# Kernel tuning notes

Measured on AMD Instinct MI355X. Metric: run time of the kernel, lower is better.

Reference implementation:

```python
import jax, jax.numpy as jnp
import numpy as np

H = 512   # hidden_dim
O = 128   # output_dim
S = 512   # max_seq_len
B = 256   # batch


def setup_inputs() -> dict:
    key = jax.random.key(0)
    ks = jax.random.split(key, 10)
    sc_ih = 1.0 / np.sqrt(H)
    inp = {
        "C": jax.random.normal(ks[0], (B, H), dtype=jnp.float32),
        "t": jax.random.uniform(ks[1], (S, B, 1), dtype=jnp.float32),
        "mask": jnp.ones((S, B), dtype=bool),
        # nn.LSTM(2H, H) params (PyTorch layout: [4H, in], gate order i,f,g,o)
        "W_ih": jax.random.uniform(ks[2], (4 * H, 2 * H), minval=-sc_ih, maxval=sc_ih),
        "W_hh": jax.random.uniform(ks[3], (4 * H, H), minval=-sc_ih, maxval=sc_ih),
        "b_ih": jax.random.uniform(ks[4], (4 * H,), minval=-sc_ih, maxval=sc_ih),
        "b_hh": jax.random.uniform(ks[5], (4 * H,), minval=-sc_ih, maxval=sc_ih),
        # nn.Linear(H, O)
        "lin_W": jax.random.uniform(ks[6], (O, H), minval=-sc_ih, maxval=sc_ih),
        "lin_b": jax.random.uniform(ks[7], (O,), minval=-sc_ih, maxval=sc_ih),
        # nn.Linear(1, H)
        "time_W": jax.random.uniform(ks[8], (H, 1), minval=-1.0, maxval=1.0),
        "time_b": jax.random.uniform(ks[9], (H,), minval=-1.0, maxval=1.0),
    }
    return inp


def _forward(C, t, W_ih, W_hh, b_ih, b_hh, lin_W, lin_b, time_W, time_b):
    # time deltas, first delta = 0   -> [S, B, 1]
    t_delta = t[1:] - t[:-1]
    t_delta_mat = jnp.concatenate([jnp.zeros_like(t_delta[0:1]), t_delta], axis=0)
    # time_lin: [S, B, H]
    time_encoded = t_delta_mat[:, :, 0:1] @ time_W.T + time_b
    # per-step LSTM input: concat(C, time_encoded[s])  -> [S, B, 2H]
    x = jnp.concatenate(
        [jnp.broadcast_to(C[None], (t.shape[0], C.shape[0], C.shape[1])), time_encoded],
        axis=-1,
    )
    # precompute input-to-gate projections in one big GEMM: [S, B, 4H]
    xg = jnp.einsum("sbi,gi->sbg", x, W_ih) + b_ih + b_hh
    Hd = C.shape[1]

    def step(carry, xg_t):
        h, c = carry
        gates = xg_t + h @ W_hh.T
        i, f, g, o = jnp.split(gates, 4, axis=-1)
        c = jax.nn.sigmoid(f) * c + jax.nn.sigmoid(i) * jnp.tanh(g)
        h = jax.nn.sigmoid(o) * jnp.tanh(c)
        return (h, c), h

    h0 = jnp.zeros((C.shape[0], Hd), dtype=C.dtype)
    _, hs = jax.lax.scan(step, (h0, h0), xg)   # hs: [S, B, H]
    return hs @ lin_W.T + lin_b                # [S, B, O]


def reference(C, t, mask, W_ih, W_hh, b_ih, b_hh, lin_W, lin_b, time_W, time_b):
    # mask is accepted by the original forward but never used
    return _forward(C, t, W_ih, W_hh, b_ih, b_hh, lin_W, lin_b, time_W, time_b)
```

## Files before the change

kernel.cpp:

```cpp
#include <hip/hip_runtime.h>
#include <stdint.h>


#define HD 512
#define BD 256
#define SD 512
#define OD 128
#define SENT 0xFF80FF80u

typedef __attribute__((ext_vector_type(8))) short short8;
typedef __attribute__((ext_vector_type(4))) float f32x4;
typedef __attribute__((ext_vector_type(4))) unsigned int u32x4;

static __device__ __forceinline__ unsigned short f2bf(float x) {
  unsigned int u = __float_as_uint(x);
  u += 0x7fffu + ((u >> 16) & 1u);
  return (unsigned short)(u >> 16);
}
static __device__ __forceinline__ float sigm(float x) {
  return 1.0f / (1.0f + __expf(-x));
}
static __device__ __forceinline__ float tanhf_(float x) {
  x = fminf(15.f, fmaxf(-15.f, x));
  float e = __expf(2.f * x);
  return (e - 1.f) / (e + 1.f);
}
static __device__ __forceinline__ int badchk(u32x4 v) {
  return (v.x == SENT) | (v.y == SENT) | (v.z == SENT) | (v.w == SENT);
}

__global__ __launch_bounds__(256) void k_cvt(const float* __restrict__ whh,
                                             const float* __restrict__ linw,
                                             unsigned short* __restrict__ whhb,
                                             unsigned short* __restrict__ linwb) {
  int i = blockIdx.x * 256 + threadIdx.x;
  whhb[i] = f2bf(whh[i]);
  if (i < OD * HD) linwb[i] = f2bf(linw[i]);
}

__global__ __launch_bounds__(256) void k_td(const float* __restrict__ t,
                                            float* __restrict__ td) {
  int i = blockIdx.x * 256 + threadIdx.x;
  float v = 0.f;
  if (i >= BD) v = t[i] - t[i - BD];
  td[i] = v;
}

__global__ __launch_bounds__(256) void k_u(const float* __restrict__ wih,
                                           const float* __restrict__ tw,
                                           const float* __restrict__ tb,
                                           const float* __restrict__ bih,
                                           const float* __restrict__ bhh,
                                           float* __restrict__ u,
                                           float* __restrict__ ub) {
  int gc = blockIdx.x * 256 + threadIdx.x;
  const float4* w4 = (const float4*)(wih + (size_t)gc * (2 * HD) + HD);
  const float4* t4 = (const float4*)tw;
  const float4* b4 = (const float4*)tb;
  float a = 0.f, b = 0.f;
  for (int k = 0; k < HD / 4; ++k) {
    float4 w = w4[k], tv = t4[k], bv = b4[k];
    a += w.x * tv.x + w.y * tv.y + w.z * tv.z + w.w * tv.w;
    b += w.x * bv.x + w.y * bv.y + w.z * bv.z + w.w * bv.w;
  }
  u[gc] = a;
  ub[gc] = b + bih[gc] + bhh[gc];
}

__global__ __launch_bounds__(1024) void k_cw(const float* __restrict__ C,
                                             const float* __restrict__ wih,
                                             const float* __restrict__ ub,
                                             float* __restrict__ CW) {
  int gc = blockIdx.x * 64 + (threadIdx.x & 63);
  int b  = blockIdx.y * 16 + (threadIdx.x >> 6);
  const float4* c4 = (const float4*)(C + (size_t)b * HD);
  const float4* w4 = (const float4*)(wih + (size_t)gc * (2 * HD));
  float acc = 0.f;
  for (int k = 0; k < HD / 4; ++k) {
    float4 cv = c4[k], wv = w4[k];
    acc += cv.x * wv.x + cv.y * wv.y + cv.z * wv.z + cv.w * wv.w;
  }
  CW[(size_t)b * (4 * HD) + gc] = acc + ub[gc];
}

__global__ __launch_bounds__(256) void k_poison(unsigned int* __restrict__ hbuf) {
  u32x4 s = {SENT, SENT, SENT, SENT};
  unsigned int* p = hbuf + (size_t)(blockIdx.x * 256 + threadIdx.x) * 4;
  asm volatile("global_store_dwordx4 %0, %1, off sc0 sc1" :: "v"(p), "v"(s) : "memory");
}

__global__ __launch_bounds__(256, 1) void k_main(
    const float* __restrict__ CW, const float* __restrict__ u,
    const float* __restrict__ td, const unsigned short* __restrict__ whhb,
    const unsigned short* __restrict__ linwb, const float* __restrict__ linb,
    unsigned short* __restrict__ hbuf, float* __restrict__ out)
{
  __shared__ __align__(16) unsigned short hlds[16 * HD];
  __shared__ __align__(16) unsigned short lwlds[16 * HD];
  __shared__ float gbuf[4][16][33];

  const int tid  = threadIdx.x;
  const int lane = tid & 63;
  const int wv   = tid >> 6;
  const int gid  = blockIdx.x & 15;
  const int m    = blockIdx.x >> 4;

  short8 w0[16], w1[16];
  {
    const unsigned short* wb =
        whhb + ((size_t)wv * HD + m * 32 + (lane & 15)) * HD + (lane >> 4) * 8;
    #pragma unroll
    for (int kk = 0; kk < 16; ++kk) {
      asm volatile("global_load_dwordx4 %0, %2, off\n\t"
                   "global_load_dwordx4 %1, %3, off"
                   : "=&v"(w0[kk]), "=&v"(w1[kk])
                   : "v"(wb + kk * 32), "v"(wb + 16 * HD + kk * 32) : "memory");
    }
  }

  if (m < 8) {
    for (int i = tid; i < 16 * 64; i += 256) {
      int rl = i >> 6, c = i & 63;
      *(short8*)((char*)lwlds + (size_t)rl * 1024 + (size_t)c * 16) =
          *(const short8*)((const char*)linwb + (size_t)(m * 16 + rl) * 1024 +
                           (size_t)((c ^ (rl & 7)) * 16));
    }
  }

  const int r    = tid >> 4;
  const int jl0  = (tid & 15) * 2;
  const int grow = gid * 16 + r;
  const int col0 = m * 32 + jl0;
  const int foff = r * 1024 + (((col0 >> 3) ^ (r & 7)) << 4) + ((col0 * 2) & 15);
  float cwr[8], ur[8];
  #pragma unroll
  for (int g = 0; g < 4; ++g) {
    int col = g * HD + col0;
    cwr[g * 2]     = CW[(size_t)grow * (4 * HD) + col];
    cwr[g * 2 + 1] = CW[(size_t)grow * (4 * HD) + col + 1];
    ur[g * 2]      = u[col];
    ur[g * 2 + 1]  = u[col + 1];
  }
  float cs0 = 0.f, cs1 = 0.f;

  const int  wsel  = 1 + (m % 3);
  const bool owsel = (m < 8) && (wv == wsel);
  float lb = 0.f;
  if (m < 8) lb = linb[m * 16 + (lane & 15)];

  char* hb = (char*)hbuf + (size_t)gid * 49152;

  const int arow  = lane & 15;
  const int akoff = lane >> 4;
  const int axor  = arow & 7;
  const int lrow  = lane & 15;
  const int lxor  = (lrow & 7) << 4;

  u32x4 v0, v1, v2, v3;
  float tdn = 0.f, tdv = 0.f;

  asm volatile("s_waitcnt vmcnt(0)" ::: "memory");
  __builtin_amdgcn_sched_barrier(0);
  __syncthreads();

  for (int t = 0; t < SD; ++t) {
    const size_t oN = (size_t)((t + 1) % 3) * 16384;
    const size_t oR = (size_t)(t % 3) * 16384;

    f32x4 acc0 = {0.f, 0.f, 0.f, 0.f}, acc1 = {0.f, 0.f, 0.f, 0.f};
    if (t > 0) {
      #pragma unroll
      for (int kk = 0; kk < 16; ++kk) {
        short8 a = *(const short8*)((const char*)hlds + (size_t)arow * 1024 +
                                    (size_t)(((kk * 4 + akoff) ^ axor) << 4));
        acc0 = __builtin_amdgcn_mfma_f32_16x16x32_bf16(a, w0[kk], acc0, 0, 0, 0);
        acc1 = __builtin_amdgcn_mfma_f32_16x16x32_bf16(a, w1[kk], acc1, 0, 0, 0);
      }
    }
    {
      int rr = (lane >> 4) * 4, cc = lane & 15;
      #pragma unroll
      for (int qq = 0; qq < 4; ++qq) {
        gbuf[wv][rr + qq][cc]      = acc0[qq];
        gbuf[wv][rr + qq][16 + cc] = acc1[qq];
      }
    }
    asm volatile("s_waitcnt lgkmcnt(0)" ::: "memory");
    __builtin_amdgcn_s_barrier();

    unsigned int hp;
    {
      float p0i = gbuf[0][r][jl0]     + cwr[0] + tdv * ur[0];
      float p1i = gbuf[0][r][jl0 + 1] + cwr[1] + tdv * ur[1];
      float p0f = gbuf[1][r][jl0]     + cwr[2] + tdv * ur[2];
      float p1f = gbuf[1][r][jl0 + 1] + cwr[3] + tdv * ur[3];
      float p0g = gbuf[2][r][jl0]     + cwr[4] + tdv * ur[4];
      float p1g = gbuf[2][r][jl0 + 1] + cwr[5] + tdv * ur[5];
      float p0o = gbuf[3][r][jl0]     + cwr[6] + tdv * ur[6];
      float p1o = gbuf[3][r][jl0 + 1] + cwr[7] + tdv * ur[7];
      cs0 = sigm(p0f) * cs0 + sigm(p0i) * tanhf_(p0g);
      cs1 = sigm(p1f) * cs1 + sigm(p1i) * tanhf_(p1g);
      float h0 = sigm(p0o) * tanhf_(cs0);
      float h1 = sigm(p1o) * tanhf_(cs1);
      hp = (unsigned int)f2bf(h0) | ((unsigned int)f2bf(h1) << 16);
    }

    {
      char* hsl = hb + oN + foff;
      asm volatile("global_store_dword %0, %1, off sc0 sc1" :: "v"(hsl), "v"(hp) : "memory");
    }

    {
      const char* src = hb + oN + (size_t)tid * 16;
      asm volatile(
          "global_load_dwordx4 %0, %4, off sc0 sc1\n\t"
          "global_load_dwordx4 %1, %5, off sc0 sc1\n\t"
          "global_load_dwordx4 %2, %6, off sc0 sc1\n\t"
          "global_load_dwordx4 %3, %7, off sc0 sc1"
          : "=&v"(v0), "=&v"(v1), "=&v"(v2), "=&v"(v3)
          : "v"(src), "v"(src + 4096), "v"(src + 8192), "v"(src + 12288)
          : "memory");
      int tt = (t + 1 < SD) ? (t + 1) : t;
      const float* ta = td + (size_t)tt * BD + grow;
      asm volatile("global_load_dword %0, %1, off" : "=&v"(tdn) : "v"(ta) : "memory");
    }

    if (owsel && t > 0) {
      f32x4 osA = {0.f, 0.f, 0.f, 0.f}, osB = {0.f, 0.f, 0.f, 0.f};
      #pragma unroll
      for (int kk = 0; kk < 8; ++kk) {
        short8 aA = *(const short8*)((const char*)hlds + (size_t)arow * 1024 +
                                     (size_t)(((kk * 4 + akoff) ^ axor) << 4));
        short8 aB = *(const short8*)((const char*)hlds + (size_t)arow * 1024 +
                                     (size_t)((((kk + 8) * 4 + akoff) ^ axor) << 4));
        short8 bA = *(const short8*)((const char*)lwlds + (size_t)lrow * 1024 +
                                     (size_t)((kk * 64 + akoff * 16) ^ lxor));
        short8 bB = *(const short8*)((const char*)lwlds + (size_t)lrow * 1024 +
                                     (size_t)(((kk + 8) * 64 + akoff * 16) ^ lxor));
        osA = __builtin_amdgcn_mfma_f32_16x16x32_bf16(aA, bA, osA, 0, 0, 0);
        osB = __builtin_amdgcn_mfma_f32_16x16x32_bf16(aB, bB, osB, 0, 0, 0);
      }
      float* ob = out + (size_t)(t - 1) * (BD * OD) + (size_t)(gid * 16) * OD + m * 16;
      int rr = (lane >> 4) * 4, cc = lane & 15;
      #pragma unroll
      for (int qq = 0; qq < 4; ++qq) {
        float vst = osA[qq] + osB[qq] + lb;
        float* oa = ob + (size_t)(rr + qq) * OD + cc;
        asm volatile("global_store_dword %0, %1, off" :: "v"(oa), "v"(vst) : "memory");
      }
    } else {
      __builtin_amdgcn_s_sleep(13);
    }

    asm volatile("s_waitcnt vmcnt(0)" ::: "memory");
    __builtin_amdgcn_sched_barrier(0);
    {
      int p0 = badchk(v0), p1 = badchk(v1), p2 = badchk(v2), p3 = badchk(v3);
      int guard = 0;
      while (p0 | p1 | p2 | p3) {
        if (++guard > (1 << 16)) break;
        __builtin_amdgcn_s_sleep(2);
        const char* src = hb + oN + (size_t)tid * 16;
        if (p0) asm volatile("global_load_dwordx4 %0, %1, off sc0 sc1" : "=&v"(v0) : "v"(src) : "memory");
        if (p1) asm volatile("global_load_dwordx4 %0, %1, off sc0 sc1" : "=&v"(v1) : "v"(src + 4096) : "memory");
        if (p2) asm volatile("global_load_dwordx4 %0, %1, off sc0 sc1" : "=&v"(v2) : "v"(src + 8192) : "memory");
        if (p3) asm volatile("global_load_dwordx4 %0, %1, off sc0 sc1" : "=&v"(v3) : "v"(src + 12288) : "memory");
        asm volatile("s_waitcnt vmcnt(0)" ::: "memory");
        __builtin_amdgcn_sched_barrier(0);
        p0 = badchk(v0); p1 = badchk(v1); p2 = badchk(v2); p3 = badchk(v3);
      }
    }

    {
      char* pp = hb + oR + (size_t)m * 1024 + (size_t)tid * 4;
      unsigned int s = SENT;
      asm volatile("global_store_dword %0, %1, off sc0 sc1" :: "v"(pp), "v"(s) : "memory");
    }

    __builtin_amdgcn_s_barrier();

    *(u32x4*)((char*)hlds + (size_t)tid * 16)         = v0;
    *(u32x4*)((char*)hlds + 4096 + (size_t)tid * 16)  = v1;
    *(u32x4*)((char*)hlds + 8192 + (size_t)tid * 16)  = v2;
    *(u32x4*)((char*)hlds + 12288 + (size_t)tid * 16) = v3;
    asm volatile("s_waitcnt lgkmcnt(0)" ::: "memory");
    __builtin_amdgcn_s_barrier();

    tdv = tdn;
  }

  if (owsel) {
    f32x4 osA = {0.f, 0.f, 0.f, 0.f}, osB = {0.f, 0.f, 0.f, 0.f};
    #pragma unroll
    for (int kk = 0; kk < 8; ++kk) {
      short8 aA = *(const short8*)((const char*)hlds + (size_t)arow * 1024 +
                                   (size_t)(((kk * 4 + akoff) ^ axor) << 4));
      short8 aB = *(const short8*)((const char*)hlds + (size_t)arow * 1024 +
                                   (size_t)((((kk + 8) * 4 + akoff) ^ axor) << 4));
      short8 bA = *(const short8*)((const char*)lwlds + (size_t)lrow * 1024 +
                                   (size_t)((kk * 64 + akoff * 16) ^ lxor));
      short8 bB = *(const short8*)((const char*)lwlds + (size_t)lrow * 1024 +
                                   (size_t)(((kk + 8) * 64 + akoff * 16) ^ lxor));
      osA = __builtin_amdgcn_mfma_f32_16x16x32_bf16(aA, bA, osA, 0, 0, 0);
      osB = __builtin_amdgcn_mfma_f32_16x16x32_bf16(aB, bB, osB, 0, 0, 0);
    }
    float* ob = out + (size_t)(SD - 1) * (BD * OD) + (size_t)(gid * 16) * OD + m * 16;
    int rr = (lane >> 4) * 4, cc = lane & 15;
    #pragma unroll
    for (int qq = 0; qq < 4; ++qq) {
      float vst = osA[qq] + osB[qq] + lb;
      float* oa = ob + (size_t)(rr + qq) * OD + cc;
      asm volatile("global_store_dword %0, %1, off" :: "v"(oa), "v"(vst) : "memory");
    }
  }
}

extern "C" void kernel_launch(void* const* d_in, const int* in_sizes, int n_in,
                              void* d_out, int out_size, void* d_ws, size_t ws_size,
                              hipStream_t stream) {
  const float* C    = (const float*)d_in[0];
  const float* t    = (const float*)d_in[1];
  const float* Wih  = (const float*)d_in[3];
  const float* Whh  = (const float*)d_in[4];
  const float* bih  = (const float*)d_in[5];
  const float* bhh  = (const float*)d_in[6];
  const float* linW = (const float*)d_in[7];
  const float* linb = (const float*)d_in[8];
  const float* tW   = (const float*)d_in[9];
  const float* tb   = (const float*)d_in[10];
  float* out = (float*)d_out;

  char* ws = (char*)d_ws;
  float*          CW    = (float*)(ws + 0);
  float*          u     = (float*)(ws + 2097152);
  float*          ub    = (float*)(ws + 2105344);
  float*          td    = (float*)(ws + 2113536);
  unsigned short* whhb  = (unsigned short*)(ws + 2637824);
  unsigned short* linwb = (unsigned short*)(ws + 4734976);
  unsigned short* hbuf  = (unsigned short*)(ws + 4866048);
  if (ws_size < 5652480) return;

  k_poison<<<192, 256, 0, stream>>>((unsigned int*)hbuf);
  k_cvt<<<4096, 256, 0, stream>>>(Whh, linW, whhb, linwb);
  k_td <<<512, 256, 0, stream>>>(t, td);
  k_u  <<<8, 256, 0, stream>>>(Wih, tW, tb, bih, bhh, u, ub);
  k_cw <<<dim3(32, 16), 1024, 0, stream>>>(C, Wih, ub, CW);
  k_main<<<256, 256, 0, stream>>>(CW, u, td, whhb, linwb, linb, hbuf, out);
}
```

Baseline: 1.856 ms.

## Stream h chunks directly from global into MFMA operands, split K across waves

Each wave now handles two gates over half of K, so partial gate sums are reduced through LDS. The wave loads its slice of the shared h-state straight from the global exchange buffer into registers in eight chunks, waiting on each chunk with a graded vmcnt so MFMAs start before the whole vector arrives. This removes the LDS staging of h and one barrier per step. The output projection is split across two waves and its store deferred by a step through a double-buffered LDS tile. It also reorders the sentinel reset, which adds per-chunk polling and more complex cross-block synchronisation.

```diff
diff --git a/kernel.cpp b/kernel.cpp
--- a/kernel.cpp
+++ b/kernel.cpp
@@ -25,9 +25,12 @@
   float e = __expf(2.f * x);
   return (e - 1.f) / (e + 1.f);
 }
-static __device__ __forceinline__ int badchk(u32x4 v) {
-  return (v.x == SENT) | (v.y == SENT) | (v.z == SENT) | (v.w == SENT);
-}
+static __device__ __forceinline__ int badchk8(short8 v) {
+  u32x4 w;
+  __builtin_memcpy(&w, &v, 16);
+  return (w.x == SENT) | (w.y == SENT) | (w.z == SENT) | (w.w == SENT);
+}
+#define KEEPALIVE(x) asm volatile("" : "+v"(x))
 
 __global__ __launch_bounds__(256) void k_cvt(const float* __restrict__ whh,
                                              const float* __restrict__ linw,
@@ -95,9 +98,9 @@
     const unsigned short* __restrict__ linwb, const float* __restrict__ linb,
     unsigned short* __restrict__ hbuf, float* __restrict__ out)
 {
-  __shared__ __align__(16) unsigned short hlds[16 * HD];
+  __shared__ float gbufP[4][2][16][33];
+  __shared__ float obufP[2][2][16][16];
   __shared__ __align__(16) unsigned short lwlds[16 * HD];
-  __shared__ float gbuf[4][16][33];
 
   const int tid  = threadIdx.x;
   const int lane = tid & 63;
@@ -105,16 +108,25 @@
   const int gid  = blockIdx.x & 15;
   const int m    = blockIdx.x >> 4;
 
-  short8 w0[16], w1[16];
+  const int ga    = (wv >> 1) * 2;
+  const int khalf = wv & 1;
+
+  short8 wA0[8], wA1[8], wB0[8], wB1[8];
   {
-    const unsigned short* wb =
-        whhb + ((size_t)wv * HD + m * 32 + (lane & 15)) * HD + (lane >> 4) * 8;
-    #pragma unroll
-    for (int kk = 0; kk < 16; ++kk) {
-      asm volatile("global_load_dwordx4 %0, %2, off\n\t"
-                   "global_load_dwordx4 %1, %3, off"
-                   : "=&v"(w0[kk]), "=&v"(w1[kk])
-                   : "v"(wb + kk * 32), "v"(wb + 16 * HD + kk * 32) : "memory");
+    #pragma unroll
+    for (int j = 0; j < 8; ++j) {
+      size_t ko = (size_t)((khalf * 8 + j) * 32 + (lane >> 4) * 8);
+      const unsigned short* pA0 =
+          whhb + (size_t)(ga * HD + m * 32 + (lane & 15)) * HD + ko;
+      const unsigned short* pB0 = pA0 + (size_t)HD * HD;
+      asm volatile(
+          "global_load_dwordx4 %0, %4, off\n\t"
+          "global_load_dwordx4 %1, %5, off\n\t"
+          "global_load_dwordx4 %2, %6, off\n\t"
+          "global_load_dwordx4 %3, %7, off"
+          : "=&v"(wA0[j]), "=&v"(wA1[j]), "=&v"(wB0[j]), "=&v"(wB1[j])
+          : "v"(pA0), "v"(pA0 + 16 * HD), "v"(pB0), "v"(pB0 + 16 * HD)
+          : "memory");
     }
   }
 
@@ -131,7 +143,6 @@
   const int jl0  = (tid & 15) * 2;
   const int grow = gid * 16 + r;
   const int col0 = m * 32 + jl0;
-  const int foff = r * 1024 + (((col0 >> 3) ^ (r & 7)) << 4) + ((col0 * 2) & 15);
   float cwr[8], ur[8];
   #pragma unroll
   for (int g = 0; g < 4; ++g) {
@@ -142,9 +153,6 @@
     ur[g * 2 + 1]  = u[col + 1];
   }
   float cs0 = 0.f, cs1 = 0.f;
-
-  const int  wsel  = 1 + (m % 3);
-  const bool owsel = (m < 8) && (wv == wsel);
   float lb = 0.f;
   if (m < 8) lb = linb[m * 16 + (lane & 15)];
 
@@ -152,52 +160,106 @@
 
   const int arow  = lane & 15;
   const int akoff = lane >> 4;
-  const int axor  = arow & 7;
+  const int aoff  = arow * 64 + akoff * 16;
   const int lrow  = lane & 15;
   const int lxor  = (lrow & 7) << 4;
-
-  u32x4 v0, v1, v2, v3;
-  float tdn = 0.f, tdv = 0.f;
-
+  const int rr    = (lane >> 4) * 4;
+  const int cc    = lane & 15;
+
+  short8 a0{}, a1{}, a2{}, a3{}, a4{}, a5{}, a6{}, a7{};
+  float  tdn = 0.f;
+
+  #pragma unroll
+  for (int i = 0; i < 8; ++i) { KEEPALIVE(cwr[i]); KEEPALIVE(ur[i]); }
+  KEEPALIVE(lb);
   asm volatile("s_waitcnt vmcnt(0)" ::: "memory");
   __builtin_amdgcn_sched_barrier(0);
   __syncthreads();
 
+#define RETRY_CHUNK(J)                                                        \
+  {                                                                           \
+    int bad = badchk8(a##J);                                                  \
+    int guard = 0;                                                            \
+    while (__any(bad)) {                                                      \
+      if (++guard > (1 << 16)) break;                                         \
+      __builtin_amdgcn_s_sleep(2);                                            \
+      if (bad)                                                                \
+        asm volatile("global_load_dwordx4 %0, %1, off sc0 sc1"               \
+                     : "=&v"(a##J) : "v"(csrc + (J) * 1024) : "memory");      \
+      asm volatile("s_waitcnt vmcnt(0)" ::: "memory");                        \
+      __builtin_amdgcn_sched_barrier(0);                                      \
+      bad = badchk8(a##J);                                                    \
+    }                                                                         \
+  }
+
+#define GATE_CHUNK(J, REMSTR)                                                 \
+  {                                                                           \
+    asm volatile("s_waitcnt vmcnt(" REMSTR ")" ::: "memory");                 \
+    __builtin_amdgcn_sched_barrier(0);                                        \
+    RETRY_CHUNK(J)                                                            \
+    accA0 = __builtin_amdgcn_mfma_f32_16x16x32_bf16(a##J, wA0[J], accA0, 0, 0, 0); \
+    accA1 = __builtin_amdgcn_mfma_f32_16x16x32_bf16(a##J, wA1[J], accA1, 0, 0, 0); \
+    accB0 = __builtin_amdgcn_mfma_f32_16x16x32_bf16(a##J, wB0[J], accB0, 0, 0, 0); \
+    accB1 = __builtin_amdgcn_mfma_f32_16x16x32_bf16(a##J, wB1[J], accB1, 0, 0, 0); \
+  }
+
+#define OP_CHUNK(J)                                                           \
+  {                                                                           \
+    short8 bf = *(const short8*)((const char*)lwlds + (size_t)lrow * 1024 +   \
+        (size_t)((((khalf * 8 + (J)) * 64 + akoff * 16)) ^ lxor));            \
+    os = __builtin_amdgcn_mfma_f32_16x16x32_bf16(a##J, bf, os, 0, 0, 0);      \
+  }
+
+#define ISSUE_CHUNK(J)                                                        \
+  asm volatile("global_load_dwordx4 %0, %1, off sc0 sc1"                      \
+               : "=&v"(a##J) : "v"(nsrc + (J) * 1024) : "memory");
+
   for (int t = 0; t < SD; ++t) {
+    const size_t oC = (size_t)(t % 3) * 16384;
     const size_t oN = (size_t)((t + 1) % 3) * 16384;
-    const size_t oR = (size_t)(t % 3) * 16384;
-
-    f32x4 acc0 = {0.f, 0.f, 0.f, 0.f}, acc1 = {0.f, 0.f, 0.f, 0.f};
+    const size_t oR = (size_t)((t + 2) % 3) * 16384;
+
+    f32x4 accA0 = {0.f, 0.f, 0.f, 0.f}, accA1 = {0.f, 0.f, 0.f, 0.f};
+    f32x4 accB0 = {0.f, 0.f, 0.f, 0.f}, accB1 = {0.f, 0.f, 0.f, 0.f};
     if (t > 0) {
-      #pragma unroll
-      for (int kk = 0; kk < 16; ++kk) {
-        short8 a = *(const short8*)((const char*)hlds + (size_t)arow * 1024 +
-                                    (size_t)(((kk * 4 + akoff) ^ axor) << 4));
-        acc0 = __builtin_amdgcn_mfma_f32_16x16x32_bf16(a, w0[kk], acc0, 0, 0, 0);
-        acc1 = __builtin_amdgcn_mfma_f32_16x16x32_bf16(a, w1[kk], acc1, 0, 0, 0);
-      }
-    }
-    {
-      int rr = (lane >> 4) * 4, cc = lane & 15;
-      #pragma unroll
-      for (int qq = 0; qq < 4; ++qq) {
-        gbuf[wv][rr + qq][cc]      = acc0[qq];
-        gbuf[wv][rr + qq][16 + cc] = acc1[qq];
-      }
+      const char* csrc = hb + oC + (size_t)(khalf * 8) * 1024 + aoff;
+      GATE_CHUNK(0, "7")
+      GATE_CHUNK(1, "6")
+      GATE_CHUNK(2, "5")
+      GATE_CHUNK(3, "4")
+      GATE_CHUNK(4, "3")
+      GATE_CHUNK(5, "2")
+      GATE_CHUNK(6, "1")
+      GATE_CHUNK(7, "0")
+    }
+
+    #pragma unroll
+    for (int qq = 0; qq < 4; ++qq) {
+      gbufP[wv][0][rr + qq][cc]      = accA0[qq];
+      gbufP[wv][0][rr + qq][16 + cc] = accA1[qq];
+      gbufP[wv][1][rr + qq][cc]      = accB0[qq];
+      gbufP[wv][1][rr + qq][16 + cc] = accB1[qq];
     }
     asm volatile("s_waitcnt lgkmcnt(0)" ::: "memory");
     __builtin_amdgcn_s_barrier();
 
+    {
+      char* pp = hb + oR + (size_t)m * 1024 + (size_t)tid * 4;
+      unsigned int s = SENT;
+      asm volatile("global_store_dword %0, %1, off sc0 sc1" :: "v"(pp), "v"(s) : "memory");
+    }
+
     unsigned int hp;
     {
-      float p0i = gbuf[0][r][jl0]     + cwr[0] + tdv * ur[0];
-      float p1i = gbuf[0][r][jl0 + 1] + cwr[1] + tdv * ur[1];
-      float p0f = gbuf[1][r][jl0]     + cwr[2] + tdv * ur[2];
-      float p1f = gbuf[1][r][jl0 + 1] + cwr[3] + tdv * ur[3];
-      float p0g = gbuf[2][r][jl0]     + cwr[4] + tdv * ur[4];
-      float p1g = gbuf[2][r][jl0 + 1] + cwr[5] + tdv * ur[5];
-      float p0o = gbuf[3][r][jl0]     + cwr[6] + tdv * ur[6];
-      float p1o = gbuf[3][r][jl0 + 1] + cwr[7] + tdv * ur[7];
+      float tdv = (t > 0) ? tdn : 0.f;
+      float p0i = gbufP[0][0][r][jl0]     + gbufP[1][0][r][jl0]     + cwr[0] + tdv * ur[0];
+      float p1i = gbufP[0][0][r][jl0 + 1] + gbufP[1][0][r][jl0 + 1] + cwr[1] + tdv * ur[1];
+      float p0f = gbufP[0][1][r][jl0]     + gbufP[1][1][r][jl0]     + cwr[2] + tdv * ur[2];
+      float p1f = gbufP[0][1][r][jl0 + 1] + gbufP[1][1][r][jl0 + 1] + cwr[3] + tdv * ur[3];
+      float p0g = gbufP[2][0][r][jl0]     + gbufP[3][0][r][jl0]     + cwr[4] + tdv * ur[4];
+      float p1g = gbufP[2][0][r][jl0 + 1] + gbufP[3][0][r][jl0 + 1] + cwr[5] + tdv * ur[5];
+      float p0o = gbufP[2][1][r][jl0]     + gbufP[3][1][r][jl0]     + cwr[6] + tdv * ur[6];
+      float p1o = gbufP[2][1][r][jl0 + 1] + gbufP[3][1][r][jl0 + 1] + cwr[7] + tdv * ur[7];
       cs0 = sigm(p0f) * cs0 + sigm(p0i) * tanhf_(p0g);
       cs1 = sigm(p1f) * cs1 + sigm(p1i) * tanhf_(p1g);
       float h0 = sigm(p0o) * tanhf_(cs0);
@@ -206,111 +268,76 @@
     }
 
     {
-      char* hsl = hb + oN + foff;
+      char* hsl = hb + oN + (size_t)m * 1024 + (size_t)(r * 64 + jl0 * 2);
       asm volatile("global_store_dword %0, %1, off sc0 sc1" :: "v"(hsl), "v"(hp) : "memory");
     }
 
-    {
-      const char* src = hb + oN + (size_t)tid * 16;
-      asm volatile(
-          "global_load_dwordx4 %0, %4, off sc0 sc1\n\t"
-          "global_load_dwordx4 %1, %5, off sc0 sc1\n\t"
-          "global_load_dwordx4 %2, %6, off sc0 sc1\n\t"
-          "global_load_dwordx4 %3, %7, off sc0 sc1"
-          : "=&v"(v0), "=&v"(v1), "=&v"(v2), "=&v"(v3)
-          : "v"(src), "v"(src + 4096), "v"(src + 8192), "v"(src + 12288)
-          : "memory");
+    const char* nsrc = hb + oN + (size_t)(khalf * 8) * 1024 + aoff;
+    if (m < 8 && wv >= 2 && t > 0) {
+      f32x4 os = {0.f, 0.f, 0.f, 0.f};
+      OP_CHUNK(0) OP_CHUNK(1) OP_CHUNK(2) OP_CHUNK(3)
+      OP_CHUNK(4) OP_CHUNK(5) OP_CHUNK(6) OP_CHUNK(7)
+      #pragma unroll
+      for (int qq = 0; qq < 4; ++qq)
+        obufP[t & 1][khalf][rr + qq][cc] = os[qq];
       int tt = (t + 1 < SD) ? (t + 1) : t;
       const float* ta = td + (size_t)tt * BD + grow;
       asm volatile("global_load_dword %0, %1, off" : "=&v"(tdn) : "v"(ta) : "memory");
-    }
-
-    if (owsel && t > 0) {
-      f32x4 osA = {0.f, 0.f, 0.f, 0.f}, osB = {0.f, 0.f, 0.f, 0.f};
-      #pragma unroll
-      for (int kk = 0; kk < 8; ++kk) {
-        short8 aA = *(const short8*)((const char*)hlds + (size_t)arow * 1024 +
-                                     (size_t)(((kk * 4 + akoff) ^ axor) << 4));
-        short8 aB = *(const short8*)((const char*)hlds + (size_t)arow * 1024 +
-                                     (size_t)((((kk + 8) * 4 + akoff) ^ axor) << 4));
-        short8 bA = *(const short8*)((const char*)lwlds + (size_t)lrow * 1024 +
-                                     (size_t)((kk * 64 + akoff * 16) ^ lxor));
-        short8 bB = *(const short8*)((const char*)lwlds + (size_t)lrow * 1024 +
-                                     (size_t)(((kk + 8) * 64 + akoff * 16) ^ lxor));
-        osA = __builtin_amdgcn_mfma_f32_16x16x32_bf16(aA, bA, osA, 0, 0, 0);
-        osB = __builtin_amdgcn_mfma_f32_16x16x32_bf16(aB, bB, osB, 0, 0, 0);
+      ISSUE_CHUNK(0) ISSUE_CHUNK(1) ISSUE_CHUNK(2) ISSUE_CHUNK(3)
+      ISSUE_CHUNK(4) ISSUE_CHUNK(5) ISSUE_CHUNK(6) ISSUE_CHUNK(7)
+    } else {
+      __builtin_amdgcn_s_sleep(4);
+      if (m < 8 && wv == 0 && t >= 2) {
+        float* ob = out + (size_t)(t - 2) * (BD * OD) + (size_t)(gid * 16) * OD + m * 16;
+        #pragma unroll
+        for (int qq = 0; qq < 4; ++qq) {
+          float v = obufP[(t - 1) & 1][0][rr + qq][cc] +
+                    obufP[(t - 1) & 1][1][rr + qq][cc] + lb;
+          float* oa = ob + (size_t)(rr + qq) * OD + cc;
+          asm volatile("global_store_dword %0, %1, off" :: "v"(oa), "v"(v) : "memory");
+        }
       }
-      float* ob = out + (size_t)(t - 1) * (BD * OD) + (size_t)(gid * 16) * OD + m * 16;
-      int rr = (lane >> 4) * 4, cc = lane & 15;
-      #pragma unroll
-      for (int qq = 0; qq < 4; ++qq) {
-        float vst = osA[qq] + osB[qq] + lb;
-        float* oa = ob + (size_t)(rr + qq) * OD + cc;
-        asm volatile("global_store_dword %0, %1, off" :: "v"(oa), "v"(vst) : "memory");
-      }
-    } else {
-      __builtin_amdgcn_s_sleep(13);
-    }
-
+      int tt = (t + 1 < SD) ? (t + 1) : t;
+      const float* ta = td + (size_t)tt * BD + grow;
+      asm volatile("global_load_dword %0, %1, off" : "=&v"(tdn) : "v"(ta) : "memory");
+      ISSUE_CHUNK(0) ISSUE_CHUNK(1) ISSUE_CHUNK(2) ISSUE_CHUNK(3)
+      ISSUE_CHUNK(4) ISSUE_CHUNK(5) ISSUE_CHUNK(6) ISSUE_CHUNK(7)
+    }
+  }
+
+  __syncthreads();
+  if (m < 8 && wv == 0) {
+    float* ob = out + (size_t)(SD - 2) * (BD * OD) + (size_t)(gid * 16) * OD + m * 16;
+    #pragma unroll
+    for (int qq = 0; qq < 4; ++qq) {
+      float v = obufP[(SD - 1) & 1][0][rr + qq][cc] +
+                obufP[(SD - 1) & 1][1][rr + qq][cc] + lb;
+      float* oa = ob + (size_t)(rr + qq) * OD + cc;
+      asm volatile("global_store_dword %0, %1, off" :: "v"(oa), "v"(v) : "memory");
+    }
+  }
+  if (m < 8 && wv >= 2) {
+    const char* csrc = hb + (size_t)(SD % 3) * 16384 + (size_t)(khalf * 8) * 1024 + aoff;
     asm volatile("s_waitcnt vmcnt(0)" ::: "memory");
     __builtin_amdgcn_sched_barrier(0);
-    {
-      int p0 = badchk(v0), p1 = badchk(v1), p2 = badchk(v2), p3 = badchk(v3);
-      int guard = 0;
-      while (p0 | p1 | p2 | p3) {
-        if (++guard > (1 << 16)) break;
-        __builtin_amdgcn_s_sleep(2);
-        const char* src = hb + oN + (size_t)tid * 16;
-        if (p0) asm volatile("global_load_dwordx4 %0, %1, off sc0 sc1" : "=&v"(v0) : "v"(src) : "memory");
-        if (p1) asm volatile("global_load_dwordx4 %0, %1, off sc0 sc1" : "=&v"(v1) : "v"(src + 4096) : "memory");
-        if (p2) asm volatile("global_load_dwordx4 %0, %1, off sc0 sc1" : "=&v"(v2) : "v"(src + 8192) : "memory");
-        if (p3) asm volatile("global_load_dwordx4 %0, %1, off sc0 sc1" : "=&v"(v3) : "v"(src + 12288) : "memory");
-        asm volatile("s_waitcnt vmcnt(0)" ::: "memory");
-        __builtin_amdgcn_sched_barrier(0);
-        p0 = badchk(v0); p1 = badchk(v1); p2 = badchk(v2); p3 = badchk(v3);
-      }
-    }
-
-    {
-      char* pp = hb + oR + (size_t)m * 1024 + (size_t)tid * 4;
-      unsigned int s = SENT;
-      asm volatile("global_store_dword %0, %1, off sc0 sc1" :: "v"(pp), "v"(s) : "memory");
-    }
-
-    __builtin_amdgcn_s_barrier();
-
-    *(u32x4*)((char*)hlds + (size_t)tid * 16)         = v0;
-    *(u32x4*)((char*)hlds + 4096 + (size_t)tid * 16)  = v1;
-    *(u32x4*)((char*)hlds + 8192 + (size_t)tid * 16)  = v2;
-    *(u32x4*)((char*)hlds + 12288 + (size_t)tid * 16) = v3;
-    asm volatile("s_waitcnt lgkmcnt(0)" ::: "memory");
-    __builtin_amdgcn_s_barrier();
-
-    tdv = tdn;
-  }
-
-  if (owsel) {
-    f32x4 osA = {0.f, 0.f, 0.f, 0.f}, osB = {0.f, 0.f, 0.f, 0.f};
-    #pragma unroll
-    for (int kk = 0; kk < 8; ++kk) {
-      short8 aA = *(const short8*)((const char*)hlds + (size_t)arow * 1024 +
-                                   (size_t)(((kk * 4 + akoff) ^ axor) << 4));
-      short8 aB = *(const short8*)((const char*)hlds + (size_t)arow * 1024 +
-                                   (size_t)((((kk + 8) * 4 + akoff) ^ axor) << 4));
-      short8 bA = *(const short8*)((const char*)lwlds + (size_t)lrow * 1024 +
-                                   (size_t)((kk * 64 + akoff * 16) ^ lxor));
-      short8 bB = *(const short8*)((const char*)lwlds + (size_t)lrow * 1024 +
-                                   (size_t)(((kk + 8) * 64 + akoff * 16) ^ lxor));
-      osA = __builtin_amdgcn_mfma_f32_16x16x32_bf16(aA, bA, osA, 0, 0, 0);
-      osB = __builtin_amdgcn_mfma_f32_16x16x32_bf16(aB, bB, osB, 0, 0, 0);
-    }
+    RETRY_CHUNK(0) RETRY_CHUNK(1) RETRY_CHUNK(2) RETRY_CHUNK(3)
+    RETRY_CHUNK(4) RETRY_CHUNK(5) RETRY_CHUNK(6) RETRY_CHUNK(7)
+    f32x4 os = {0.f, 0.f, 0.f, 0.f};
+    OP_CHUNK(0) OP_CHUNK(1) OP_CHUNK(2) OP_CHUNK(3)
+    OP_CHUNK(4) OP_CHUNK(5) OP_CHUNK(6) OP_CHUNK(7)
+    #pragma unroll
+    for (int qq = 0; qq < 4; ++qq)
+      obufP[SD & 1][khalf][rr + qq][cc] = os[qq];
+  }
+  __syncthreads();
+  if (m < 8 && wv == 0) {
     float* ob = out + (size_t)(SD - 1) * (BD * OD) + (size_t)(gid * 16) * OD + m * 16;
-    int rr = (lane >> 4) * 4, cc = lane & 15;
     #pragma unroll
     for (int qq = 0; qq < 4; ++qq) {
-      float vst = osA[qq] + osB[qq] + lb;
+      float v = obufP[SD & 1][0][rr + qq][cc] +
+                obufP[SD & 1][1][rr + qq][cc] + lb;
       float* oa = ob + (size_t)(rr + qq) * OD + cc;
-      asm volatile("global_store_dword %0, %1, off" :: "v"(oa), "v"(vst) : "memory");
+      asm volatile("global_store_dword %0, %1, off" :: "v"(oa), "v"(v) : "memory");
     }
   }
 }
```

Result: slower. 2.076 ms (+11.8%).

## Specialize waves for h exchange and double-buffer LDS hidden state

Applied to the files above, without the earlier changes.

Reworks the per-step cross-block exchange of the hidden state. Each block now gathers its new h tile in LDS and one wave writes it to global with wide stores and re-poisons the stale slot. Two waves poll for and load the peers' h into a double-buffered LDS copy, while another wave computes the output projection. The goal is fewer barriers and less serialized global traffic per timestep. The cost is more LDS, harder wait-count reasoning, and added risk in the sentinel-poll protocol.

```diff
diff --git a/kernel.cpp b/kernel.cpp
--- a/kernel.cpp
+++ b/kernel.cpp
@@ -25,9 +25,12 @@
   float e = __expf(2.f * x);
   return (e - 1.f) / (e + 1.f);
 }
-static __device__ __forceinline__ int badchk(u32x4 v) {
-  return (v.x == SENT) | (v.y == SENT) | (v.z == SENT) | (v.w == SENT);
-}
+static __device__ __forceinline__ int badchk8(short8 v) {
+  u32x4 w;
+  __builtin_memcpy(&w, &v, 16);
+  return (w.x == SENT) | (w.y == SENT) | (w.z == SENT) | (w.w == SENT);
+}
+#define KEEPALIVE(x) asm volatile("" : "+v"(x))
 
 __global__ __launch_bounds__(256) void k_cvt(const float* __restrict__ whh,
                                              const float* __restrict__ linw,
@@ -95,8 +98,9 @@
     const unsigned short* __restrict__ linwb, const float* __restrict__ linb,
     unsigned short* __restrict__ hbuf, float* __restrict__ out)
 {
-  __shared__ __align__(16) unsigned short hlds[16 * HD];
+  __shared__ __align__(16) unsigned short hlds[2][16 * HD];
   __shared__ __align__(16) unsigned short lwlds[16 * HD];
+  __shared__ __align__(16) unsigned short hcell[16 * 32];
   __shared__ float gbuf[4][16][33];
 
   const int tid  = threadIdx.x;
@@ -131,7 +135,6 @@
   const int jl0  = (tid & 15) * 2;
   const int grow = gid * 16 + r;
   const int col0 = m * 32 + jl0;
-  const int foff = r * 1024 + (((col0 >> 3) ^ (r & 7)) << 4) + ((col0 * 2) & 15);
   float cwr[8], ur[8];
   #pragma unroll
   for (int g = 0; g < 4; ++g) {
@@ -142,9 +145,6 @@
     ur[g * 2 + 1]  = u[col + 1];
   }
   float cs0 = 0.f, cs1 = 0.f;
-
-  const int  wsel  = 1 + (m % 3);
-  const bool owsel = (m < 8) && (wv == wsel);
   float lb = 0.f;
   if (m < 8) lb = linb[m * 16 + (lane & 15)];
 
@@ -155,23 +155,32 @@
   const int axor  = arow & 7;
   const int lrow  = lane & 15;
   const int lxor  = (lrow & 7) << 4;
-
-  u32x4 v0, v1, v2, v3;
-  float tdn = 0.f, tdv = 0.f;
-
+  const int srow   = lane >> 2;
+  const int sj     = lane & 3;
+  const int sboff  = srow * 1024 + (((m * 4 + sj) ^ (srow & 7)) << 4);
+
+  short8 a0{}, a1{}, a2{}, a3{}, a4{}, a5{}, a6{}, a7{};
+  float  tdn = 0.f, tdv = 0.f;
+  u32x4  sv = {SENT, SENT, SENT, SENT};
+
+  #pragma unroll
+  for (int i = 0; i < 8; ++i) { KEEPALIVE(cwr[i]); KEEPALIVE(ur[i]); }
+  KEEPALIVE(lb);
   asm volatile("s_waitcnt vmcnt(0)" ::: "memory");
   __builtin_amdgcn_sched_barrier(0);
   __syncthreads();
 
   for (int t = 0; t < SD; ++t) {
     const size_t oN = (size_t)((t + 1) % 3) * 16384;
-    const size_t oR = (size_t)(t % 3) * 16384;
+    const size_t oR = (size_t)((t + 2) % 3) * 16384;
+    const int cur = t & 1, nxt = cur ^ 1;
+    const char* hcur = (const char*)&hlds[cur][0];
 
     f32x4 acc0 = {0.f, 0.f, 0.f, 0.f}, acc1 = {0.f, 0.f, 0.f, 0.f};
     if (t > 0) {
       #pragma unroll
       for (int kk = 0; kk < 16; ++kk) {
-        short8 a = *(const short8*)((const char*)hlds + (size_t)arow * 1024 +
+        short8 a = *(const short8*)(hcur + (size_t)arow * 1024 +
                                     (size_t)(((kk * 4 + akoff) ^ axor) << 4));
         acc0 = __builtin_amdgcn_mfma_f32_16x16x32_bf16(a, w0[kk], acc0, 0, 0, 0);
         acc1 = __builtin_amdgcn_mfma_f32_16x16x32_bf16(a, w1[kk], acc1, 0, 0, 0);
@@ -188,7 +197,11 @@
     asm volatile("s_waitcnt lgkmcnt(0)" ::: "memory");
     __builtin_amdgcn_s_barrier();
 
-    unsigned int hp;
+    if (wv == 2)      asm volatile("s_waitcnt vmcnt(0)" ::: "memory");
+    else if (wv == 3) asm volatile("s_waitcnt vmcnt(2)" ::: "memory");
+    __builtin_amdgcn_sched_barrier(0);
+    tdv = (t > 0) ? tdn : 0.f;
+
     {
       float p0i = gbuf[0][r][jl0]     + cwr[0] + tdv * ur[0];
       float p1i = gbuf[0][r][jl0 + 1] + cwr[1] + tdv * ur[1];
@@ -202,100 +215,127 @@
       cs1 = sigm(p1f) * cs1 + sigm(p1i) * tanhf_(p1g);
       float h0 = sigm(p0o) * tanhf_(cs0);
       float h1 = sigm(p1o) * tanhf_(cs1);
-      hp = (unsigned int)f2bf(h0) | ((unsigned int)f2bf(h1) << 16);
-    }
-
-    {
-      char* hsl = hb + oN + foff;
-      asm volatile("global_store_dword %0, %1, off sc0 sc1" :: "v"(hsl), "v"(hp) : "memory");
-    }
-
-    {
-      const char* src = hb + oN + (size_t)tid * 16;
-      asm volatile(
-          "global_load_dwordx4 %0, %4, off sc0 sc1\n\t"
-          "global_load_dwordx4 %1, %5, off sc0 sc1\n\t"
-          "global_load_dwordx4 %2, %6, off sc0 sc1\n\t"
-          "global_load_dwordx4 %3, %7, off sc0 sc1"
-          : "=&v"(v0), "=&v"(v1), "=&v"(v2), "=&v"(v3)
-          : "v"(src), "v"(src + 4096), "v"(src + 8192), "v"(src + 12288)
-          : "memory");
-      int tt = (t + 1 < SD) ? (t + 1) : t;
-      const float* ta = td + (size_t)tt * BD + grow;
-      asm volatile("global_load_dword %0, %1, off" : "=&v"(tdn) : "v"(ta) : "memory");
-    }
-
-    if (owsel && t > 0) {
-      f32x4 osA = {0.f, 0.f, 0.f, 0.f}, osB = {0.f, 0.f, 0.f, 0.f};
-      #pragma unroll
-      for (int kk = 0; kk < 8; ++kk) {
-        short8 aA = *(const short8*)((const char*)hlds + (size_t)arow * 1024 +
-                                     (size_t)(((kk * 4 + akoff) ^ axor) << 4));
-        short8 aB = *(const short8*)((const char*)hlds + (size_t)arow * 1024 +
-                                     (size_t)((((kk + 8) * 4 + akoff) ^ axor) << 4));
-        short8 bA = *(const short8*)((const char*)lwlds + (size_t)lrow * 1024 +
-                                     (size_t)((kk * 64 + akoff * 16) ^ lxor));
-        short8 bB = *(const short8*)((const char*)lwlds + (size_t)lrow * 1024 +
-                                     (size_t)(((kk + 8) * 64 + akoff * 16) ^ lxor));
-        osA = __builtin_amdgcn_mfma_f32_16x16x32_bf16(aA, bA, osA, 0, 0, 0);
-        osB = __builtin_amdgcn_mfma_f32_16x16x32_bf16(aB, bB, osB, 0, 0, 0);
-      }
-      float* ob = out + (size_t)(t - 1) * (BD * OD) + (size_t)(gid * 16) * OD + m * 16;
-      int rr = (lane >> 4) * 4, cc = lane & 15;
-      #pragma unroll
-      for (int qq = 0; qq < 4; ++qq) {
-        float vst = osA[qq] + osB[qq] + lb;
-        float* oa = ob + (size_t)(rr + qq) * OD + cc;
-        asm volatile("global_store_dword %0, %1, off" :: "v"(oa), "v"(vst) : "memory");
-      }
-    } else {
-      __builtin_amdgcn_s_sleep(13);
-    }
-
-    asm volatile("s_waitcnt vmcnt(0)" ::: "memory");
-    __builtin_amdgcn_sched_barrier(0);
-    {
-      int p0 = badchk(v0), p1 = badchk(v1), p2 = badchk(v2), p3 = badchk(v3);
-      int guard = 0;
-      while (p0 | p1 | p2 | p3) {
-        if (++guard > (1 << 16)) break;
-        __builtin_amdgcn_s_sleep(2);
-        const char* src = hb + oN + (size_t)tid * 16;
-        if (p0) asm volatile("global_load_dwordx4 %0, %1, off sc0 sc1" : "=&v"(v0) : "v"(src) : "memory");
-        if (p1) asm volatile("global_load_dwordx4 %0, %1, off sc0 sc1" : "=&v"(v1) : "v"(src + 4096) : "memory");
-        if (p2) asm volatile("global_load_dwordx4 %0, %1, off sc0 sc1" : "=&v"(v2) : "v"(src + 8192) : "memory");
-        if (p3) asm volatile("global_load_dwordx4 %0, %1, off sc0 sc1" : "=&v"(v3) : "v"(src + 12288) : "memory");
-        asm volatile("s_waitcnt vmcnt(0)" ::: "memory");
-        __builtin_amdgcn_sched_barrier(0);
-        p0 = badchk(v0); p1 = badchk(v1); p2 = badchk(v2); p3 = badchk(v3);
-      }
-    }
-
-    {
-      char* pp = hb + oR + (size_t)m * 1024 + (size_t)tid * 4;
-      unsigned int s = SENT;
-      asm volatile("global_store_dword %0, %1, off sc0 sc1" :: "v"(pp), "v"(s) : "memory");
-    }
-
-    __builtin_amdgcn_s_barrier();
-
-    *(u32x4*)((char*)hlds + (size_t)tid * 16)         = v0;
-    *(u32x4*)((char*)hlds + 4096 + (size_t)tid * 16)  = v1;
-    *(u32x4*)((char*)hlds + 8192 + (size_t)tid * 16)  = v2;
-    *(u32x4*)((char*)hlds + 12288 + (size_t)tid * 16) = v3;
+      unsigned int hp = (unsigned int)f2bf(h0) | ((unsigned int)f2bf(h1) << 16);
+      *(unsigned int*)((char*)hcell + (size_t)(r * 64) + (size_t)(jl0 * 2)) = hp;
+    }
     asm volatile("s_waitcnt lgkmcnt(0)" ::: "memory");
     __builtin_amdgcn_s_barrier();
 
-    tdv = tdn;
-  }
-
-  if (owsel) {
+    if (wv == 3) {
+      asm volatile("s_waitcnt vmcnt(0)" ::: "memory");
+      __builtin_amdgcn_sched_barrier(0);
+      u32x4 hv = *(const u32x4*)((const char*)hcell + (size_t)lane * 16);
+      asm volatile("s_waitcnt lgkmcnt(0)" ::: "memory");
+      __builtin_amdgcn_sched_barrier(0);
+      {
+        int tt = (t + 1 < SD) ? (t + 1) : t;
+        const float* ta = td + (size_t)tt * BD + grow;
+        asm volatile("global_load_dword %0, %1, off" : "=&v"(tdn) : "v"(ta) : "memory");
+      }
+      asm volatile("global_store_dwordx4 %0, %1, off sc0 sc1"
+                   :: "v"(hb + oN + sboff), "v"(hv) : "memory");
+      asm volatile("global_store_dwordx4 %0, %1, off sc0 sc1"
+                   :: "v"(hb + oR + sboff), "v"(sv) : "memory");
+    } else if (wv == 2) {
+      if (m < 8 && t > 0) {
+        f32x4 osA = {0.f, 0.f, 0.f, 0.f}, osB = {0.f, 0.f, 0.f, 0.f};
+        #pragma unroll
+        for (int kk = 0; kk < 8; ++kk) {
+          short8 aA = *(const short8*)(hcur + (size_t)arow * 1024 +
+                                       (size_t)(((kk * 4 + akoff) ^ axor) << 4));
+          short8 aB = *(const short8*)(hcur + (size_t)arow * 1024 +
+                                       (size_t)((((kk + 8) * 4 + akoff) ^ axor) << 4));
+          short8 bA = *(const short8*)((const char*)lwlds + (size_t)lrow * 1024 +
+                                       (size_t)((kk * 64 + akoff * 16) ^ lxor));
+          short8 bB = *(const short8*)((const char*)lwlds + (size_t)lrow * 1024 +
+                                       (size_t)(((kk + 8) * 64 + akoff * 16) ^ lxor));
+          osA = __builtin_amdgcn_mfma_f32_16x16x32_bf16(aA, bA, osA, 0, 0, 0);
+          osB = __builtin_amdgcn_mfma_f32_16x16x32_bf16(aB, bB, osB, 0, 0, 0);
+        }
+        float* ob = out + (size_t)(t - 1) * (BD * OD) + (size_t)(gid * 16) * OD + m * 16;
+        int rr = (lane >> 4) * 4, cc = lane & 15;
+        #pragma unroll
+        for (int qq = 0; qq < 4; ++qq) {
+          float vst = osA[qq] + osB[qq] + lb;
+          float* oa = ob + (size_t)(rr + qq) * OD + cc;
+          asm volatile("global_store_dword %0, %1, off" :: "v"(oa), "v"(vst) : "memory");
+        }
+      }
+      {
+        int tt = (t + 1 < SD) ? (t + 1) : t;
+        const float* ta = td + (size_t)tt * BD + grow;
+        asm volatile("global_load_dword %0, %1, off" : "=&v"(tdn) : "v"(ta) : "memory");
+      }
+    } else {
+      __builtin_amdgcn_s_sleep(6);
+      {
+        int tt = (t + 1 < SD) ? (t + 1) : t;
+        const float* ta = td + (size_t)tt * BD + grow;
+        asm volatile("global_load_dword %0, %1, off" : "=&v"(tdn) : "v"(ta) : "memory");
+      }
+      const char* nsrc = hb + oN + (size_t)(wv * 8) * 1024 + (size_t)lane * 16;
+      asm volatile(
+          "global_load_dwordx4 %0, %8, off sc0 sc1\n\t"
+          "global_load_dwordx4 %1, %9, off sc0 sc1\n\t"
+          "global_load_dwordx4 %2, %10, off sc0 sc1\n\t"
+          "global_load_dwordx4 %3, %11, off sc0 sc1\n\t"
+          "global_load_dwordx4 %4, %12, off sc0 sc1\n\t"
+          "global_load_dwordx4 %5, %13, off sc0 sc1\n\t"
+          "global_load_dwordx4 %6, %14, off sc0 sc1\n\t"
+          "global_load_dwordx4 %7, %15, off sc0 sc1\n\t"
+          "s_waitcnt vmcnt(0)"
+          : "=&v"(a0), "=&v"(a1), "=&v"(a2), "=&v"(a3),
+            "=&v"(a4), "=&v"(a5), "=&v"(a6), "=&v"(a7)
+          : "v"(nsrc), "v"(nsrc + 1024), "v"(nsrc + 2048), "v"(nsrc + 3072),
+            "v"(nsrc + 4096), "v"(nsrc + 5120), "v"(nsrc + 6144), "v"(nsrc + 7168)
+          : "memory");
+      __builtin_amdgcn_sched_barrier(0);
+      {
+        int b0 = badchk8(a0), b1 = badchk8(a1), b2 = badchk8(a2), b3 = badchk8(a3);
+        int b4 = badchk8(a4), b5 = badchk8(a5), b6 = badchk8(a6), b7 = badchk8(a7);
+        int guard = 0;
+        while (__any(b0 | b1 | b2 | b3 | b4 | b5 | b6 | b7)) {
+          if (++guard > (1 << 16)) break;
+          __builtin_amdgcn_s_sleep(2);
+          if (b0) asm volatile("global_load_dwordx4 %0, %1, off sc0 sc1" : "=&v"(a0) : "v"(nsrc) : "memory");
+          if (b1) asm volatile("global_load_dwordx4 %0, %1, off sc0 sc1" : "=&v"(a1) : "v"(nsrc + 1024) : "memory");
+          if (b2) asm volatile("global_load_dwordx4 %0, %1, off sc0 sc1" : "=&v"(a2) : "v"(nsrc + 2048) : "memory");
+          if (b3) asm volatile("global_load_dwordx4 %0, %1, off sc0 sc1" : "=&v"(a3) : "v"(nsrc + 3072) : "memory");
+          if (b4) asm volatile("global_load_dwordx4 %0, %1, off sc0 sc1" : "=&v"(a4) : "v"(nsrc + 4096) : "memory");
+          if (b5) asm volatile("global_load_dwordx4 %0, %1, off sc0 sc1" : "=&v"(a5) : "v"(nsrc + 5120) : "memory");
+          if (b6) asm volatile("global_load_dwordx4 %0, %1, off sc0 sc1" : "=&v"(a6) : "v"(nsrc + 6144) : "memory");
+          if (b7) asm volatile("global_load_dwordx4 %0, %1, off sc0 sc1" : "=&v"(a7) : "v"(nsrc + 7168) : "memory");
+          asm volatile("s_waitcnt vmcnt(0)" ::: "memory");
+          __builtin_amdgcn_sched_barrier(0);
+          b0 = badchk8(a0); b1 = badchk8(a1); b2 = badchk8(a2); b3 = badchk8(a3);
+          b4 = badchk8(a4); b5 = badchk8(a5); b6 = badchk8(a6); b7 = badchk8(a7);
+        }
+      }
+      {
+        char* dst = (char*)&hlds[nxt][0] + (size_t)(wv * 8) * 1024 + (size_t)lane * 16;
+        *(short8*)(dst)        = a0;
+        *(short8*)(dst + 1024) = a1;
+        *(short8*)(dst + 2048) = a2;
+        *(short8*)(dst + 3072) = a3;
+        *(short8*)(dst + 4096) = a4;
+        *(short8*)(dst + 5120) = a5;
+        *(short8*)(dst + 6144) = a6;
+        *(short8*)(dst + 7168) = a7;
+      }
+    }
+
+    asm volatile("s_waitcnt lgkmcnt(0)" ::: "memory");
+    __builtin_amdgcn_s_barrier();
+  }
+
+  if (wv == 2 && m < 8) {
+    const char* hcur = (const char*)&hlds[SD & 1][0];
     f32x4 osA = {0.f, 0.f, 0.f, 0.f}, osB = {0.f, 0.f, 0.f, 0.f};
     #pragma unroll
     for (int kk = 0; kk < 8; ++kk) {
-      short8 aA = *(const short8*)((const char*)hlds + (size_t)arow * 1024 +
+      short8 aA = *(const short8*)(hcur + (size_t)arow * 1024 +
                                    (size_t)(((kk * 4 + akoff) ^ axor) << 4));
-      short8 aB = *(const short8*)((const char*)hlds + (size_t)arow * 1024 +
+      short8 aB = *(const short8*)(hcur + (size_t)arow * 1024 +
                                    (size_t)((((kk + 8) * 4 + akoff) ^ axor) << 4));
       short8 bA = *(const short8*)((const char*)lwlds + (size_t)lrow * 1024 +
                                    (size_t)((kk * 64 + akoff * 16) ^ lxor));
```

After: 1.712 ms. 1.08x faster.
